# Optimization experiments

Measured on AMD Instinct MI355X. Metric: run time of the kernel, lower is better.

## Reference

```python
import jax, jax.numpy as jnp
import numpy as np

B, L, D = 8, 4096, 1024


def setup_inputs() -> dict:
    key = jax.random.key(0)
    k1, k2, k3 = jax.random.split(key, 3)
    states = jax.random.normal(k1, (B, L, D), dtype=jnp.float32)
    reasoning_mask = jax.random.randint(k2, (B, L), 0, 2).astype(jnp.float32)
    result_token_positions = jax.random.randint(k3, (B,), 0, L, dtype=jnp.int64)
    return {
        "states": states,
        "reasoning_mask": reasoning_mask,
        "result_token_positions": result_token_positions,
    }


def reference(states, reasoning_mask, result_token_positions):
    # states: [B, L, D]; reasoning_mask: [B, L]; result_token_positions: [B]
    Bs, Ls, Ds = states.shape
    # ||s_t - s_{t-1}||  -> [B, L-1]
    deltas = jnp.linalg.norm(states[:, 1:, :] - states[:, :-1, :], axis=-1)
    # relu of consecutive delta increase -> [B, L-2]
    delta_increase = jax.nn.relu(deltas[:, 1:] - deltas[:, :-1])
    mask = reasoning_mask[:, 2:]  # [B, L-2]
    # approach weight: dist = max(rp - t - 2, 0); weight = 2 + (5-dist)*0.5 if dist < 5 else 1
    t = jnp.arange(Ls - 2)
    dist = jnp.maximum(result_token_positions[:, None] - t[None, :] - 2, 0)  # [B, L-2]
    approach_weight = jnp.where(
        dist < 5,
        jnp.float32(2.0) + (5 - dist).astype(states.dtype) * jnp.float32(0.5),
        jnp.float32(1.0),
    )
    weighted = delta_increase * mask * approach_weight
    return weighted.sum() / (mask.sum() + 1e-9)
```

## Files before the change

kernel.cpp:

```cpp
#include <hip/hip_runtime.h>
#include <math.h>

#define BB 8
#define LL 4096
#define DD 1024
#define LM1 4095
#define LM2 4094
#define CHUNK 16
#define NDELTA 17
#define ROWS 18
#define NCH 256
#define NBLK 512

__global__ __launch_bounds__(256) void fused_kernel(const float* __restrict__ states,
                                                    const float* __restrict__ rmask,
                                                    const int* __restrict__ rpos,
                                                    float* __restrict__ pnum,
                                                    float* __restrict__ pden) {
    const int tid = threadIdx.x;
    const int lane = tid & 63;
    const int wid = tid >> 6;
    const int w = blockIdx.x * 4 + wid;
    const int b = w >> 8;
    const int c = w & (NCH - 1);
    const int t0 = c * CHUNK;

    const float4* base = (const float4*)states + (size_t)b * (LL * (DD / 4)) + lane;

    float partial[NDELTA];

    float4 p0, p1, p2, p3;
    {
        const float4* rp_ = base + (size_t)t0 * (DD / 4);
        p0 = rp_[0]; p1 = rp_[64]; p2 = rp_[128]; p3 = rp_[192];
    }
    #pragma unroll
    for (int r = 1; r < ROWS; ++r) {
        int row = t0 + r;
        if (row > LL - 1) row = LL - 1;
        const float4* rp_ = base + (size_t)row * (DD / 4);
        float4 c0 = rp_[0], c1 = rp_[64], c2 = rp_[128], c3 = rp_[192];
        float s = 0.0f, d;
        d = c0.x - p0.x; s += d * d;
        d = c0.y - p0.y; s += d * d;
        d = c0.z - p0.z; s += d * d;
        d = c0.w - p0.w; s += d * d;
        d = c1.x - p1.x; s += d * d;
        d = c1.y - p1.y; s += d * d;
        d = c1.z - p1.z; s += d * d;
        d = c1.w - p1.w; s += d * d;
        d = c2.x - p2.x; s += d * d;
        d = c2.y - p2.y; s += d * d;
        d = c2.z - p2.z; s += d * d;
        d = c2.w - p2.w; s += d * d;
        d = c3.x - p3.x; s += d * d;
        d = c3.y - p3.y; s += d * d;
        d = c3.z - p3.z; s += d * d;
        d = c3.w - p3.w; s += d * d;
        partial[r - 1] = s;
        p0 = c0; p1 = c1; p2 = c2; p3 = c3;
    }

    float dval = 0.0f;
    #pragma unroll
    for (int d2 = 0; d2 < NDELTA; ++d2) {
        float s = partial[d2];
        #pragma unroll
        for (int off = 1; off < 64; off <<= 1) s += __shfl_xor(s, off);
        if (lane == d2) dval = sqrtf(s);
    }
    float dnext = __shfl_down(dval, 1);

    const int t = t0 + lane;
    const bool valid = (lane < CHUNK) && (t < LM2);
    float inc = dnext - dval;
    inc = inc > 0.0f ? inc : 0.0f;
    int midx = b * LL + t + 2;
    if (midx > BB * LL - 1) midx = BB * LL - 1;
    float m = valid ? rmask[midx] : 0.0f;
    const int rp = rpos[b];
    int dist = rp - t - 2;
    if (dist < 0) dist = 0;
    const float wgt = (dist < 5) ? (2.0f + (float)(5 - dist) * 0.5f) : 1.0f;
    float num = valid ? inc * m * wgt : 0.0f;
    float den = m;

    #pragma unroll
    for (int off = 32; off > 0; off >>= 1) {
        num += __shfl_down(num, off);
        den += __shfl_down(den, off);
    }
    __shared__ float ln[4], ld[4];
    if (lane == 0) { ln[wid] = num; ld[wid] = den; }
    __syncthreads();
    if (tid == 0) {
        pnum[blockIdx.x] = ln[0] + ln[1] + ln[2] + ln[3];
        pden[blockIdx.x] = ld[0] + ld[1] + ld[2] + ld[3];
    }
}

__global__ __launch_bounds__(512) void final_kernel(const float* __restrict__ pnum,
                                                    const float* __restrict__ pden,
                                                    float* __restrict__ out) {
    const int tid = threadIdx.x;
    const int lane = tid & 63;
    const int wid = tid >> 6;
    float n = pnum[tid];
    float d = pden[tid];
    #pragma unroll
    for (int off = 32; off > 0; off >>= 1) {
        n += __shfl_down(n, off);
        d += __shfl_down(d, off);
    }
    __shared__ float ln[8], ld[8];
    if (lane == 0) { ln[wid] = n; ld[wid] = d; }
    __syncthreads();
    if (tid == 0) {
        float N = 0.0f, D = 0.0f;
        #pragma unroll
        for (int i = 0; i < 8; ++i) { N += ln[i]; D += ld[i]; }
        out[0] = N / (D + 1e-9f);
    }
}

extern "C" void kernel_launch(void* const* d_in, const int* in_sizes, int n_in,
                              void* d_out, int out_size, void* d_ws, size_t ws_size,
                              hipStream_t stream) {
    const float* states = (const float*)d_in[0];
    const float* rmask  = (const float*)d_in[1];
    const int*   rpos   = (const int*)d_in[2];
    float* out = (float*)d_out;

    float* ws   = (float*)d_ws;
    float* pnum = ws;
    float* pden = ws + NBLK;

    fused_kernel<<<NBLK, 256, 0, stream>>>(states, rmask, rpos, pnum, pden);
    final_kernel<<<1, 512, 0, stream>>>(pnum, pden, out);
}
```

Before: 199.8 us.

## Split hidden dim across waves and double row chunk per block

Each block now covers 32 consecutive rows, with its four waves each handling a quarter of the hidden dimension, and partial squared sums are combined through shared memory. This halves the halo row overhead per chunk and doubles the block count, with launch bounds hinting higher occupancy. In exchange, each wave performs more cross-lane reductions (33 per wave), adds a block barrier, and the final reduction grows to 1024 entries.

```diff
diff --git a/kernel.cpp b/kernel.cpp
--- a/kernel.cpp
+++ b/kernel.cpp
@@ -4,104 +4,92 @@
 #define BB 8
 #define LL 4096
 #define DD 1024
-#define LM1 4095
 #define LM2 4094
-#define CHUNK 16
-#define NDELTA 17
-#define ROWS 18
-#define NCH 256
-#define NBLK 512
+#define CHUNK 32
+#define NDELTA 33
+#define ROWS 34
+#define NCH 128
+#define NBLK (BB * NCH)
 
-__global__ __launch_bounds__(256) void fused_kernel(const float* __restrict__ states,
-                                                    const float* __restrict__ rmask,
-                                                    const int* __restrict__ rpos,
-                                                    float* __restrict__ pnum,
-                                                    float* __restrict__ pden) {
+__global__ __launch_bounds__(256, 4) void fused_kernel(const float* __restrict__ states,
+                                                       const float* __restrict__ rmask,
+                                                       const int* __restrict__ rpos,
+                                                       float* __restrict__ pnum,
+                                                       float* __restrict__ pden) {
     const int tid = threadIdx.x;
     const int lane = tid & 63;
     const int wid = tid >> 6;
-    const int w = blockIdx.x * 4 + wid;
-    const int b = w >> 8;
-    const int c = w & (NCH - 1);
+    const int b = blockIdx.x >> 7;
+    const int c = blockIdx.x & (NCH - 1);
     const int t0 = c * CHUNK;
 
-    const float4* base = (const float4*)states + (size_t)b * (LL * (DD / 4)) + lane;
+    const float4* base = (const float4*)states + (size_t)b * (LL * (DD / 4)) + wid * 64 + lane;
 
     float partial[NDELTA];
 
-    float4 p0, p1, p2, p3;
-    {
-        const float4* rp_ = base + (size_t)t0 * (DD / 4);
-        p0 = rp_[0]; p1 = rp_[64]; p2 = rp_[128]; p3 = rp_[192];
-    }
+    float4 p = base[(size_t)t0 * (DD / 4)];
     #pragma unroll
     for (int r = 1; r < ROWS; ++r) {
         int row = t0 + r;
         if (row > LL - 1) row = LL - 1;
-        const float4* rp_ = base + (size_t)row * (DD / 4);
-        float4 c0 = rp_[0], c1 = rp_[64], c2 = rp_[128], c3 = rp_[192];
+        float4 cur = base[(size_t)row * (DD / 4)];
         float s = 0.0f, d;
-        d = c0.x - p0.x; s += d * d;
-        d = c0.y - p0.y; s += d * d;
-        d = c0.z - p0.z; s += d * d;
-        d = c0.w - p0.w; s += d * d;
-        d = c1.x - p1.x; s += d * d;
-        d = c1.y - p1.y; s += d * d;
-        d = c1.z - p1.z; s += d * d;
-        d = c1.w - p1.w; s += d * d;
-        d = c2.x - p2.x; s += d * d;
-        d = c2.y - p2.y; s += d * d;
-        d = c2.z - p2.z; s += d * d;
-        d = c2.w - p2.w; s += d * d;
-        d = c3.x - p3.x; s += d * d;
-        d = c3.y - p3.y; s += d * d;
-        d = c3.z - p3.z; s += d * d;
-        d = c3.w - p3.w; s += d * d;
+        d = cur.x - p.x; s += d * d;
+        d = cur.y - p.y; s += d * d;
+        d = cur.z - p.z; s += d * d;
+        d = cur.w - p.w; s += d * d;
         partial[r - 1] = s;
-        p0 = c0; p1 = c1; p2 = c2; p3 = c3;
+        p = cur;
     }
 
-    float dval = 0.0f;
+    float qs = 0.0f;
     #pragma unroll
     for (int d2 = 0; d2 < NDELTA; ++d2) {
         float s = partial[d2];
         #pragma unroll
         for (int off = 1; off < 64; off <<= 1) s += __shfl_xor(s, off);
-        if (lane == d2) dval = sqrtf(s);
+        if (lane == d2) qs = s;
     }
-    float dnext = __shfl_down(dval, 1);
 
-    const int t = t0 + lane;
-    const bool valid = (lane < CHUNK) && (t < LM2);
-    float inc = dnext - dval;
-    inc = inc > 0.0f ? inc : 0.0f;
-    int midx = b * LL + t + 2;
-    if (midx > BB * LL - 1) midx = BB * LL - 1;
-    float m = valid ? rmask[midx] : 0.0f;
-    const int rp = rpos[b];
-    int dist = rp - t - 2;
-    if (dist < 0) dist = 0;
-    const float wgt = (dist < 5) ? (2.0f + (float)(5 - dist) * 0.5f) : 1.0f;
-    float num = valid ? inc * m * wgt : 0.0f;
-    float den = m;
+    __shared__ float qsum[4][NDELTA];
+    if (lane < NDELTA) qsum[wid][lane] = qs;
+    __syncthreads();
 
-    #pragma unroll
-    for (int off = 32; off > 0; off >>= 1) {
-        num += __shfl_down(num, off);
-        den += __shfl_down(den, off);
-    }
-    __shared__ float ln[4], ld[4];
-    if (lane == 0) { ln[wid] = num; ld[wid] = den; }
-    __syncthreads();
-    if (tid == 0) {
-        pnum[blockIdx.x] = ln[0] + ln[1] + ln[2] + ln[3];
-        pden[blockIdx.x] = ld[0] + ld[1] + ld[2] + ld[3];
+    if (wid == 0) {
+        float dval = 0.0f;
+        if (lane < NDELTA)
+            dval = sqrtf(qsum[0][lane] + qsum[1][lane] + qsum[2][lane] + qsum[3][lane]);
+        float dnext = __shfl_down(dval, 1);
+
+        const int t = t0 + lane;
+        const bool valid = (lane < CHUNK) && (t < LM2);
+        float inc = dnext - dval;
+        inc = inc > 0.0f ? inc : 0.0f;
+        int midx = b * LL + t + 2;
+        if (midx > BB * LL - 1) midx = BB * LL - 1;
+        float m = valid ? rmask[midx] : 0.0f;
+        const int rp = rpos[b];
+        int dist = rp - t - 2;
+        if (dist < 0) dist = 0;
+        const float wgt = (dist < 5) ? (2.0f + (float)(5 - dist) * 0.5f) : 1.0f;
+        float num = valid ? inc * m * wgt : 0.0f;
+        float den = m;
+
+        #pragma unroll
+        for (int off = 32; off > 0; off >>= 1) {
+            num += __shfl_down(num, off);
+            den += __shfl_down(den, off);
+        }
+        if (lane == 0) {
+            pnum[blockIdx.x] = num;
+            pden[blockIdx.x] = den;
+        }
     }
 }
 
-__global__ __launch_bounds__(512) void final_kernel(const float* __restrict__ pnum,
-                                                    const float* __restrict__ pden,
-                                                    float* __restrict__ out) {
+__global__ __launch_bounds__(1024) void final_kernel(const float* __restrict__ pnum,
+                                                     const float* __restrict__ pden,
+                                                     float* __restrict__ out) {
     const int tid = threadIdx.x;
     const int lane = tid & 63;
     const int wid = tid >> 6;
@@ -112,13 +100,13 @@
         n += __shfl_down(n, off);
         d += __shfl_down(d, off);
     }
-    __shared__ float ln[8], ld[8];
+    __shared__ float ln[16], ld[16];
     if (lane == 0) { ln[wid] = n; ld[wid] = d; }
     __syncthreads();
     if (tid == 0) {
         float N = 0.0f, D = 0.0f;
         #pragma unroll
-        for (int i = 0; i < 8; ++i) { N += ln[i]; D += ld[i]; }
+        for (int i = 0; i < 16; ++i) { N += ln[i]; D += ld[i]; }
         out[0] = N / (D + 1e-9f);
     }
 }
@@ -136,5 +124,5 @@
     float* pden = ws + NBLK;
 
     fused_kernel<<<NBLK, 256, 0, stream>>>(states, rmask, rpos, pnum, pden);
-    final_kernel<<<1, 512, 0, stream>>>(pnum, pden, out);
+    final_kernel<<<1, 1024, 0, stream>>>(pnum, pden, out);
 }
```

Result: faster. 195.7 us (-2.1%).
